# Kernel tuning notes

Hardware: AMD Instinct MI355X
Metric: run time of the kernel (lower is better)

Reference implementation:

```python
import jax, jax.numpy as jnp
import numpy as np

B, S, F = 2, 2048, 2048
H, D = 16, 128  # F == H * D


def setup_inputs() -> dict:
    key = jax.random.key(0)
    k1, k2, k3 = jax.random.split(key, 3)
    x = jax.random.normal(k1, (B, S, F), dtype=jnp.float32)
    # causal attention mask, broadcast over batch and heads
    mask = jnp.tril(jnp.ones((S, S), dtype=bool))[None, None, :, :]
    init_std = 0.02
    c_attn_kernel = jax.random.normal(k2, (F, 3 * F), dtype=jnp.float32) * init_std
    c_attn_bias = jnp.zeros((3 * F,), dtype=jnp.float32)
    c_proj_kernel = jax.random.normal(k3, (F, F), dtype=jnp.float32) * init_std
    c_proj_bias = jnp.zeros((F,), dtype=jnp.float32)
    return {
        "x": x,
        "mask": mask,
        "c_attn_kernel": c_attn_kernel,
        "c_attn_bias": c_attn_bias,
        "c_proj_kernel": c_proj_kernel,
        "c_proj_bias": c_proj_bias,
    }


def reference(x, mask, c_attn_kernel, c_attn_bias, c_proj_kernel, c_proj_bias):
    dtype = x.dtype
    # fused QKV projection: [B,S,F] @ [F,3F] -> [B,S,3F]
    hidden = jnp.einsum('bsf,fe->bse', x, c_attn_kernel) + c_attn_bias
    q, k, v = jnp.split(hidden, 3, axis=-1)
    split = lambda t: t.reshape(t.shape[:-1] + (H, D))  # [B,S,H,D]
    q, k, v = split(q), split(k), split(v)
    q = q / jnp.sqrt(jnp.asarray(D, dtype))
    scores = jnp.einsum('bqhd,bkhd->bhqk', q, k)  # [B,H,S,S]
    big_neg = jnp.finfo(dtype).min
    scores = jnp.where(mask[..., :S, :S], scores, big_neg)
    weights = jax.nn.softmax(scores, axis=-1)
    z = jnp.einsum('bhqk,bkhd->bqhd', weights, v)  # [B,S,H,D]
    merged = z.reshape(z.shape[:-2] + (F,))  # [B,S,F]
    out = jnp.einsum('bsf,fe->bse', merged, c_proj_kernel) + c_proj_bias
    return out
```

## Files before the change

### kernel.cpp

```cpp
#include <hip/hip_runtime.h>
#include <hip/hip_bf16.h>
#include <stdint.h>

typedef __attribute__((ext_vector_type(8))) __bf16 bf16x8;
typedef __attribute__((ext_vector_type(4))) __bf16 bf16x4;
typedef __attribute__((ext_vector_type(4))) float f32x4;

#define DEV __device__ __forceinline__

static constexpr int S = 2048, F = 2048, H = 16, D = 128;
static constexpr int KDIM = F;
static constexpr float QSCALE = 0.08838834764831845f;

DEV void gll16(const void* g, void* l) {
  __builtin_amdgcn_global_load_lds(
      (const __attribute__((address_space(1))) void*)g,
      (__attribute__((address_space(3))) void*)l, 16, 0, 0);
}

DEV f32x4 mfma16(bf16x8 a, bf16x8 b, f32x4 c) {
  return __builtin_amdgcn_mfma_f32_16x16x32_bf16(a, b, c, 0, 0, 0);
}

extern __shared__ char smem[];

__global__ void k_cvt(const float* __restrict__ in, __bf16* __restrict__ out) {
  int i = blockIdx.x * 256 + threadIdx.x;
  float4 v = reinterpret_cast<const float4*>(in)[i];
  bf16x4 o = {(__bf16)v.x, (__bf16)v.y, (__bf16)v.z, (__bf16)v.w};
  reinterpret_cast<bf16x4*>(out)[i] = o;
}

__global__ void k_transpose(const float* __restrict__ in, __bf16* __restrict__ out,
                            int rows, int cols) {
  __shared__ float t[64][65];
  const int c0 = blockIdx.x * 64, r0 = blockIdx.y * 64;
  const int tx = threadIdx.x & 63, ty = threadIdx.x >> 6;
#pragma unroll
  for (int i = 0; i < 64; i += 4)
    t[ty + i][tx] = in[(size_t)(r0 + ty + i) * cols + c0 + tx];
  __syncthreads();
#pragma unroll
  for (int i = 0; i < 64; i += 4)
    out[(size_t)(c0 + ty + i) * rows + r0 + tx] = (__bf16)t[tx][ty + i];
}

template <int EPI>
__global__ __launch_bounds__(512, 2) void k_gemm_tb(
    const __bf16* __restrict__ A, const __bf16* __restrict__ Bt,
    const float* __restrict__ bias,
    __bf16* __restrict__ qo, __bf16* __restrict__ ko, __bf16* __restrict__ vo,
    float* __restrict__ fo, int nbx) {
  const int tid = threadIdx.x;
  const int lane = tid & 63, wid = tid >> 6;
  const int wm = wid >> 2, wn = wid & 3;
  const int ln = lane & 15, lm = lane >> 4;

  const int q8 = gridDim.x >> 3;
  const int lin = (blockIdx.x & 7) * q8 + (blockIdx.x >> 3);
  const int bx = lin % nbx, by = lin / nbx;
  const int mBase = by * 128, nBase = bx * 256;

  int srcA[2], dstA[2], srcB[4], dstB[4];
#pragma unroll
  for (int j = 0; j < 2; ++j) {
    int c = j * 512 + tid, r = c >> 3, cc = c & 7;
    srcA[j] = r * KDIM + ((cc ^ (r & 7)) << 3);
    dstA[j] = j * 8192 + wid * 1024;
  }
#pragma unroll
  for (int j = 0; j < 4; ++j) {
    int c = j * 512 + tid, r = c >> 3, cc = c & 7;
    srcB[j] = r * KDIM + ((cc ^ (r & 7)) << 3);
    dstB[j] = 16384 + j * 8192 + wid * 1024;
  }
  const __bf16* Ab = A + (size_t)mBase * KDIM;
  const __bf16* Bb = Bt + (size_t)nBase * KDIM;

  int loA[2], loB[2];
#pragma unroll
  for (int ks = 0; ks < 2; ++ks) {
    int slot = (ks * 4 + lm) ^ (ln & 7);
    loA[ks] = (wm * 64 + ln) * 128 + slot * 16;
    loB[ks] = 16384 + (wn * 64 + ln) * 128 + slot * 16;
  }

  f32x4 acc[4][4] = {};
  constexpr int NT = KDIM / 64;

#pragma unroll
  for (int j = 0; j < 2; ++j) gll16(Ab + srcA[j], smem + dstA[j]);
#pragma unroll
  for (int j = 0; j < 4; ++j) gll16(Bb + srcB[j], smem + dstB[j]);
#pragma unroll
  for (int j = 0; j < 2; ++j) gll16(Ab + 64 + srcA[j], smem + 49152 + dstA[j]);
#pragma unroll
  for (int j = 0; j < 4; ++j) gll16(Bb + 64 + srcB[j], smem + 49152 + dstB[j]);
  asm volatile("s_waitcnt vmcnt(6)" ::: "memory");
  __builtin_amdgcn_s_barrier();
  __builtin_amdgcn_sched_barrier(0);

  for (int t = 0; t < NT; ++t) {
    const char* cbuf = smem + (t % 3) * 49152;
    char* nbuf = smem + ((t + 2) % 3) * 49152;
    const __bf16* Asrc = Ab + (t + 2) * 64;
    const __bf16* Bsrc = Bb + (t + 2) * 64;
    const bool pf = (t + 2 < NT);

    bf16x8 af0[4], bf0[4];
#pragma unroll
    for (int mi = 0; mi < 4; ++mi)
      af0[mi] = *reinterpret_cast<const bf16x8*>(cbuf + mi * 2048 + loA[0]);
#pragma unroll
    for (int ni = 0; ni < 4; ++ni)
      bf0[ni] = *reinterpret_cast<const bf16x8*>(cbuf + ni * 2048 + loB[0]);
    if (pf) {
      gll16(Asrc + srcA[0], nbuf + dstA[0]);
      gll16(Asrc + srcA[1], nbuf + dstA[1]);
      gll16(Bsrc + srcB[0], nbuf + dstB[0]);
    }
    __builtin_amdgcn_s_setprio(1);
#pragma unroll
    for (int mi = 0; mi < 4; ++mi)
#pragma unroll
      for (int ni = 0; ni < 4; ++ni)
        acc[mi][ni] = mfma16(af0[mi], bf0[ni], acc[mi][ni]);
    __builtin_amdgcn_s_setprio(0);

    bf16x8 af1[4], bf1[4];
#pragma unroll
    for (int mi = 0; mi < 4; ++mi)
      af1[mi] = *reinterpret_cast<const bf16x8*>(cbuf + mi * 2048 + loA[1]);
#pragma unroll
    for (int ni = 0; ni < 4; ++ni)
      bf1[ni] = *reinterpret_cast<const bf16x8*>(cbuf + ni * 2048 + loB[1]);
    if (pf) {
      gll16(Bsrc + srcB[1], nbuf + dstB[1]);
      gll16(Bsrc + srcB[2], nbuf + dstB[2]);
      gll16(Bsrc + srcB[3], nbuf + dstB[3]);
    }
    __builtin_amdgcn_s_setprio(1);
#pragma unroll
    for (int mi = 0; mi < 4; ++mi)
#pragma unroll
      for (int ni = 0; ni < 4; ++ni)
        acc[mi][ni] = mfma16(af1[mi], bf1[ni], acc[mi][ni]);
    __builtin_amdgcn_s_setprio(0);

    if (t < NT - 2)
      asm volatile("s_waitcnt vmcnt(6) lgkmcnt(0)" ::: "memory");
    else
      asm volatile("s_waitcnt vmcnt(0) lgkmcnt(0)" ::: "memory");
    __builtin_amdgcn_s_barrier();
    __builtin_amdgcn_sched_barrier(0);
  }

  if (EPI == 0) {
    const int sec = nBase >> 11;
#pragma unroll
    for (int mi = 0; mi < 4; ++mi) {
      const int grow = mBase + wm * 64 + mi * 16 + lm * 4;
      const int b = grow >> 11, s0 = grow & 2047;
#pragma unroll
      for (int ni = 0; ni < 4; ++ni) {
        const int gcol = nBase + wn * 64 + ni * 16 + ln;
        const float bv = bias[gcol];
        const int h = (gcol >> 7) & 15, d = gcol & 127;
        const int bh = b * H + h;
        if (sec == 0) {
#pragma unroll
          for (int r = 0; r < 4; ++r)
            qo[((size_t)bh * S + s0 + r) * D + d] = (__bf16)((acc[mi][ni][r] + bv) * QSCALE);
        } else if (sec == 1) {
#pragma unroll
          for (int r = 0; r < 4; ++r)
            ko[((size_t)bh * S + s0 + r) * D + d] = (__bf16)(acc[mi][ni][r] + bv);
        } else {
          bf16x4 pv = {(__bf16)(acc[mi][ni][0] + bv), (__bf16)(acc[mi][ni][1] + bv),
                       (__bf16)(acc[mi][ni][2] + bv), (__bf16)(acc[mi][ni][3] + bv)};
          *reinterpret_cast<bf16x4*>(vo + ((size_t)bh * D + d) * S + s0) = pv;
        }
      }
    }
  } else {
#pragma unroll
    for (int mi = 0; mi < 4; ++mi) {
      const int grow = mBase + wm * 64 + mi * 16 + lm * 4;
#pragma unroll
      for (int ni = 0; ni < 4; ++ni) {
        const int gcol = nBase + wn * 64 + ni * 16 + ln;
        const float bv = bias[gcol];
#pragma unroll
        for (int r = 0; r < 4; ++r)
          fo[(size_t)(grow + r) * F + gcol] = acc[mi][ni][r] + bv;
      }
    }
  }
}

__global__ __launch_bounds__(256, 2) void k_attn(
    const __bf16* __restrict__ qb, const __bf16* __restrict__ kb,
    const __bf16* __restrict__ vtb, __bf16* __restrict__ zb) {
  const int lane = threadIdx.x & 63, w = threadIdx.x >> 6;
  const int lm = lane >> 4, ln = lane & 15;
  const int blk = blockIdx.x;
  const int bh = blk & 31;
  const int qt = 15 - (blk >> 5);
  const int qw = qt * 128 + w * 32;

  const __bf16* qp = qb + (size_t)bh * S * D;
  const __bf16* kp = kb + (size_t)bh * S * D;
  const __bf16* vp = vtb + (size_t)bh * D * S;
  char* pw = smem + 65536 + w * 4096;

  int ksrc[4], kdst[4], vsrc[4], vdst[4];
#pragma unroll
  for (int j = 0; j < 4; ++j) {
    int c = (w * 4 + j) * 64 + lane;
    int kr = c >> 4, kps = (c & 15) ^ (kr & 7);
    ksrc[j] = kr * D + kps * 8;
    kdst[j] = (w * 4 + j) * 1024;
    int vr = c >> 3, vps = (c & 7) ^ (vr & 7);
    vsrc[j] = vr * S + vps * 8;
    vdst[j] = 16384 + (w * 4 + j) * 1024;
  }

  bf16x8 qf[2][4];
#pragma unroll
  for (int mi = 0; mi < 2; ++mi)
#pragma unroll
    for (int kf = 0; kf < 4; ++kf)
      qf[mi][kf] = *reinterpret_cast<const bf16x8*>(qp + (qw + mi * 16 + ln) * D + kf * 32 + lm * 8);

  f32x4 Oa[2][8] = {};
  float mrow[2][4], lrow[2][4];
#pragma unroll
  for (int mi = 0; mi < 2; ++mi)
#pragma unroll
    for (int r = 0; r < 4; ++r) { mrow[mi][r] = -3.0e38f; lrow[mi][r] = 0.0f; }

  const int ktEnd = 2 * qt + 1;

#pragma unroll
  for (int j = 0; j < 4; ++j) gll16(kp + ksrc[j], smem + kdst[j]);
#pragma unroll
  for (int j = 0; j < 4; ++j) gll16(vp + vsrc[j], smem + vdst[j]);
  asm volatile("s_waitcnt vmcnt(0)" ::: "memory");
  __builtin_amdgcn_s_barrier();
  __builtin_amdgcn_sched_barrier(0);

  for (int kt = 0; kt <= ktEnd; ++kt) {
    const int kv0 = kt * 64;
    const int cur = kt & 1;

    if (kt < ktEnd) {
      const int nk = (kt + 1) * 64;
      char* nbuf = smem + (cur ^ 1) * 32768;
#pragma unroll
      for (int j = 0; j < 4; ++j) gll16(kp + (size_t)nk * D + ksrc[j], nbuf + kdst[j]);
#pragma unroll
      for (int j = 0; j < 4; ++j) gll16(vp + nk + vsrc[j], nbuf + vdst[j] - 16384 + 16384);
    }

    if (kv0 <= qw + 31) {
      const char* Kb = smem + cur * 32768;
      const char* Vb = Kb + 16384;
      const bool diag = (kv0 + 63 > qw);

      f32x4 sacc[2][4] = {};
#pragma unroll
      for (int kf = 0; kf < 4; ++kf) {
        bf16x8 kfr[4];
#pragma unroll
        for (int ni = 0; ni < 4; ++ni) {
          int row = ni * 16 + ln;
          int ch = (kf * 4 + lm) ^ (row & 7);
          kfr[ni] = *reinterpret_cast<const bf16x8*>(Kb + row * 256 + ch * 16);
        }
        __builtin_amdgcn_s_setprio(1);
#pragma unroll
        for (int mi = 0; mi < 2; ++mi)
#pragma unroll
          for (int ni = 0; ni < 4; ++ni)
            sacc[mi][ni] = mfma16(qf[mi][kf], kfr[ni], sacc[mi][ni]);
        __builtin_amdgcn_s_setprio(0);
      }

      if (diag) {
#pragma unroll
        for (int ni = 0; ni < 4; ++ni) {
          int c = kv0 + ni * 16 + ln;
#pragma unroll
          for (int mi = 0; mi < 2; ++mi) {
            int q0r = qw + mi * 16 + lm * 4;
#pragma unroll
            for (int r = 0; r < 4; ++r)
              if (c > q0r + r) sacc[mi][ni][r] = -1e30f;
          }
        }
      }

#pragma unroll
      for (int mi = 0; mi < 2; ++mi)
#pragma unroll
        for (int r = 0; r < 4; ++r) {
          float mx = fmaxf(fmaxf(sacc[mi][0][r], sacc[mi][1][r]),
                           fmaxf(sacc[mi][2][r], sacc[mi][3][r]));
          mx = fmaxf(mx, __shfl_xor(mx, 1, 64));
          mx = fmaxf(mx, __shfl_xor(mx, 2, 64));
          mx = fmaxf(mx, __shfl_xor(mx, 4, 64));
          mx = fmaxf(mx, __shfl_xor(mx, 8, 64));
          float mnew = fmaxf(mrow[mi][r], mx);
          float corr = __expf(mrow[mi][r] - mnew);
          mrow[mi][r] = mnew;
          float rs = 0.0f;
#pragma unroll
          for (int ni = 0; ni < 4; ++ni) {
            float p = __expf(sacc[mi][ni][r] - mnew);
            sacc[mi][ni][r] = p;
            rs += p;
          }
          lrow[mi][r] = lrow[mi][r] * corr + rs;
#pragma unroll
          for (int ni = 0; ni < 8; ++ni) Oa[mi][ni][r] *= corr;
        }

#pragma unroll
      for (int mi = 0; mi < 2; ++mi)
#pragma unroll
        for (int ni = 0; ni < 4; ++ni)
#pragma unroll
          for (int r = 0; r < 4; ++r) {
            int row = mi * 16 + lm * 4 + r;
            int bo = (row * 128 + (ni * 16 + ln) * 2) ^ ((row & 7) << 4);
            *reinterpret_cast<__bf16*>(pw + bo) = (__bf16)sacc[mi][ni][r];
          }

      asm volatile("s_waitcnt lgkmcnt(0)" ::: "memory");
      __builtin_amdgcn_sched_barrier(0);

#pragma unroll
      for (int kf = 0; kf < 2; ++kf) {
        bf16x8 pfr[2], vfr[8];
#pragma unroll
        for (int mi = 0; mi < 2; ++mi) {
          int row = mi * 16 + ln;
          int ch = (kf * 4 + lm) ^ (row & 7);
          pfr[mi] = *reinterpret_cast<const bf16x8*>(pw + row * 128 + ch * 16);
        }
#pragma unroll
        for (int ni = 0; ni < 8; ++ni) {
          int row = ni * 16 + ln;
          int ch = (kf * 4 + lm) ^ (row & 7);
          vfr[ni] = *reinterpret_cast<const bf16x8*>(Vb + row * 128 + ch * 16);
        }
        __builtin_amdgcn_s_setprio(1);
#pragma unroll
        for (int mi = 0; mi < 2; ++mi)
#pragma unroll
          for (int ni = 0; ni < 8; ++ni)
            Oa[mi][ni] = mfma16(pfr[mi], vfr[ni], Oa[mi][ni]);
        __builtin_amdgcn_s_setprio(0);
      }
    }

    asm volatile("s_waitcnt vmcnt(0) lgkmcnt(0)" ::: "memory");
    __builtin_amdgcn_s_barrier();
    __builtin_amdgcn_sched_barrier(0);
  }

#pragma unroll
  for (int mi = 0; mi < 2; ++mi)
#pragma unroll
    for (int r = 0; r < 4; ++r) {
      float ls = lrow[mi][r];
      ls += __shfl_xor(ls, 1, 64);
      ls += __shfl_xor(ls, 2, 64);
      ls += __shfl_xor(ls, 4, 64);
      ls += __shfl_xor(ls, 8, 64);
      lrow[mi][r] = 1.0f / ls;
    }
  const int b = bh >> 4, h = bh & 15;
#pragma unroll
  for (int mi = 0; mi < 2; ++mi)
#pragma unroll
    for (int ni = 0; ni < 8; ++ni) {
      int d = ni * 16 + ln;
#pragma unroll
      for (int r = 0; r < 4; ++r) {
        int qrow = qw + mi * 16 + lm * 4 + r;
        zb[(size_t)(b * S + qrow) * F + h * D + d] = (__bf16)(Oa[mi][ni][r] * lrow[mi][r]);
      }
    }
}

extern "C" void kernel_launch(void* const* d_in, const int* in_sizes, int n_in,
                              void* d_out, int out_size, void* d_ws, size_t ws_size,
                              hipStream_t stream) {
  const float* x = (const float*)d_in[0];
  const float* w_attn = (const float*)d_in[2];
  const float* b_attn = (const float*)d_in[3];
  const float* w_proj = (const float*)d_in[4];
  const float* b_proj = (const float*)d_in[5];
  float* out = (float*)d_out;

  char* ws = (char*)d_ws;
  __bf16* xb    = (__bf16*)(ws + 0);
  __bf16* wqkv  = (__bf16*)(ws + 16777216);
  __bf16* wpro  = (__bf16*)(ws + 41943040);
  __bf16* qb    = (__bf16*)(ws + 50331648);
  __bf16* kb    = (__bf16*)(ws + 67108864);
  __bf16* vtb   = (__bf16*)(ws + 83886080);
  __bf16* zb    = xb;

  (void)hipFuncSetAttribute((const void*)k_gemm_tb<0>,
                            hipFuncAttributeMaxDynamicSharedMemorySize, 147456);
  (void)hipFuncSetAttribute((const void*)k_gemm_tb<1>,
                            hipFuncAttributeMaxDynamicSharedMemorySize, 147456);
  (void)hipFuncSetAttribute((const void*)k_attn,
                            hipFuncAttributeMaxDynamicSharedMemorySize, 81920);

  k_cvt<<<8192, 256, 0, stream>>>(x, xb);
  k_transpose<<<dim3(96, 32), 256, 0, stream>>>(w_attn, wqkv, 2048, 6144);
  k_transpose<<<dim3(32, 32), 256, 0, stream>>>(w_proj, wpro, 2048, 2048);
  k_gemm_tb<0><<<768, 512, 147456, stream>>>(xb, wqkv, b_attn, qb, kb, vtb, nullptr, 24);
  k_attn<<<512, 256, 81920, stream>>>(qb, kb, vtb, zb);
  k_gemm_tb<1><<<256, 512, 147456, stream>>>(zb, wpro, b_proj, nullptr, nullptr, nullptr, out, 8);
}
```

Before: 274.5 us.

## Use dedicated 256x384-tile QKV GEMM kernel with one wave of blocks

After: 275.1 us. Within noise of the previous version (+0.2%).

```diff
diff --git a/kernel.cpp b/kernel.cpp
--- a/kernel.cpp
+++ b/kernel.cpp
@@ -45,12 +45,136 @@
     out[(size_t)(c0 + ty + i) * rows + r0 + tx] = (__bf16)t[tx][ty + i];
 }
 
-template <int EPI>
-__global__ __launch_bounds__(512, 2) void k_gemm_tb(
+__global__ __launch_bounds__(512, 2) void k_qkv(
     const __bf16* __restrict__ A, const __bf16* __restrict__ Bt,
     const float* __restrict__ bias,
-    __bf16* __restrict__ qo, __bf16* __restrict__ ko, __bf16* __restrict__ vo,
-    float* __restrict__ fo, int nbx) {
+    __bf16* __restrict__ qo, __bf16* __restrict__ ko, __bf16* __restrict__ vo) {
+  const int tid = threadIdx.x;
+  const int lane = tid & 63, wid = tid >> 6;
+  const int wm = wid >> 2, wn = wid & 3;
+  const int ln = lane & 15, lm = lane >> 4;
+
+  const int lin = (blockIdx.x & 7) * 32 + (blockIdx.x >> 3);
+  const int by = lin >> 4, bx = lin & 15;
+  const int mBase = by * 256, nBase = bx * 384;
+
+  const int r0 = tid >> 3, cc = tid & 7;
+  const int src0 = r0 * KDIM + ((cc ^ (r0 & 7)) << 3);
+  const __bf16* Ab = A + (size_t)mBase * KDIM + src0;
+  const __bf16* Bb = Bt + (size_t)nBase * KDIM + src0;
+  const int dstBase = wid * 1024;
+
+  int rA[2], rB[2];
+#pragma unroll
+  for (int ks = 0; ks < 2; ++ks) {
+    const int slot = (ks * 4 + lm) ^ (ln & 7);
+    rA[ks] = (wm * 128 + ln) * 128 + slot * 16;
+    rB[ks] = 32768 + (wn * 96 + ln) * 128 + slot * 16;
+  }
+
+  f32x4 acc[8][6] = {};
+  constexpr int NT = KDIM / 64;
+
+#pragma unroll
+  for (int j = 0; j < 4; ++j) gll16(Ab + j * 131072, smem + j * 8192 + dstBase);
+#pragma unroll
+  for (int j = 0; j < 6; ++j) gll16(Bb + j * 131072, smem + 32768 + j * 8192 + dstBase);
+  asm volatile("s_waitcnt vmcnt(0)" ::: "memory");
+  __builtin_amdgcn_s_barrier();
+  __builtin_amdgcn_sched_barrier(0);
+
+  for (int t = 0; t < NT; ++t) {
+    const int cur = t & 1;
+    const char* cb = smem + cur * 81920;
+    char* nb = smem + (cur ^ 1) * 81920;
+    const __bf16* An = Ab + (t + 1) * 64;
+    const __bf16* Bn = Bb + (t + 1) * 64;
+    const bool pf = (t + 1 < NT);
+
+    {
+      bf16x8 a[8], b[6];
+#pragma unroll
+      for (int mi = 0; mi < 8; ++mi)
+        a[mi] = *reinterpret_cast<const bf16x8*>(cb + rA[0] + mi * 2048);
+#pragma unroll
+      for (int ni = 0; ni < 6; ++ni)
+        b[ni] = *reinterpret_cast<const bf16x8*>(cb + rB[0] + ni * 2048);
+      if (pf) {
+#pragma unroll
+        for (int j = 0; j < 4; ++j) gll16(An + j * 131072, nb + j * 8192 + dstBase);
+#pragma unroll
+        for (int j = 0; j < 2; ++j) gll16(Bn + j * 131072, nb + 32768 + j * 8192 + dstBase);
+      }
+      asm volatile("s_waitcnt lgkmcnt(0)" ::: "memory");
+      __builtin_amdgcn_sched_barrier(0);
+      __builtin_amdgcn_s_setprio(1);
+#pragma unroll
+      for (int ni = 0; ni < 6; ++ni)
+#pragma unroll
+        for (int mi = 0; mi < 8; ++mi)
+          acc[mi][ni] = mfma16(a[mi], b[ni], acc[mi][ni]);
+      __builtin_amdgcn_s_setprio(0);
+    }
+
+    {
+      bf16x8 a[8], b[6];
+#pragma unroll
+      for (int mi = 0; mi < 8; ++mi)
+        a[mi] = *reinterpret_cast<const bf16x8*>(cb + rA[1] + mi * 2048);
+#pragma unroll
+      for (int ni = 0; ni < 6; ++ni)
+        b[ni] = *reinterpret_cast<const bf16x8*>(cb + rB[1] + ni * 2048);
+      if (pf) {
+#pragma unroll
+        for (int j = 2; j < 6; ++j) gll16(Bn + j * 131072, nb + 32768 + j * 8192 + dstBase);
+      }
+      asm volatile("s_waitcnt lgkmcnt(0)" ::: "memory");
+      __builtin_amdgcn_sched_barrier(0);
+      __builtin_amdgcn_s_setprio(1);
+#pragma unroll
+      for (int ni = 0; ni < 6; ++ni)
+#pragma unroll
+        for (int mi = 0; mi < 8; ++mi)
+          acc[mi][ni] = mfma16(a[mi], b[ni], acc[mi][ni]);
+      __builtin_amdgcn_s_setprio(0);
+    }
+
+    asm volatile("s_waitcnt vmcnt(0)" ::: "memory");
+    __builtin_amdgcn_s_barrier();
+    __builtin_amdgcn_sched_barrier(0);
+  }
+
+#pragma unroll
+  for (int mi = 0; mi < 8; ++mi) {
+    const int grow = mBase + wm * 128 + mi * 16 + lm * 4;
+    const int b = grow >> 11, s0 = grow & 2047;
+#pragma unroll
+    for (int ni = 0; ni < 6; ++ni) {
+      const int gcol = nBase + wn * 96 + ni * 16 + ln;
+      const float bv = bias[gcol];
+      const int sec = gcol >> 11;
+      const int h = (gcol >> 7) & 15, d = gcol & 127;
+      const int bh = b * H + h;
+      if (sec == 0) {
+#pragma unroll
+        for (int r = 0; r < 4; ++r)
+          qo[((size_t)bh * S + s0 + r) * D + d] = (__bf16)((acc[mi][ni][r] + bv) * QSCALE);
+      } else if (sec == 1) {
+#pragma unroll
+        for (int r = 0; r < 4; ++r)
+          ko[((size_t)bh * S + s0 + r) * D + d] = (__bf16)(acc[mi][ni][r] + bv);
+      } else {
+        bf16x4 pv = {(__bf16)(acc[mi][ni][0] + bv), (__bf16)(acc[mi][ni][1] + bv),
+                     (__bf16)(acc[mi][ni][2] + bv), (__bf16)(acc[mi][ni][3] + bv)};
+        *reinterpret_cast<bf16x4*>(vo + ((size_t)bh * D + d) * S + s0) = pv;
+      }
+    }
+  }
+}
+
+__global__ __launch_bounds__(512, 2) void k_proj(
+    const __bf16* __restrict__ A, const __bf16* __restrict__ Bt,
+    const float* __restrict__ bias, float* __restrict__ fo, int nbx) {
   const int tid = threadIdx.x;
   const int lane = tid & 63, wid = tid >> 6;
   const int wm = wid >> 2, wn = wid & 3;
@@ -155,45 +279,16 @@
     __builtin_amdgcn_sched_barrier(0);
   }
 
-  if (EPI == 0) {
-    const int sec = nBase >> 11;
-#pragma unroll
-    for (int mi = 0; mi < 4; ++mi) {
-      const int grow = mBase + wm * 64 + mi * 16 + lm * 4;
-      const int b = grow >> 11, s0 = grow & 2047;
-#pragma unroll
-      for (int ni = 0; ni < 4; ++ni) {
-        const int gcol = nBase + wn * 64 + ni * 16 + ln;
-        const float bv = bias[gcol];
-        const int h = (gcol >> 7) & 15, d = gcol & 127;
-        const int bh = b * H + h;
-        if (sec == 0) {
-#pragma unroll
-          for (int r = 0; r < 4; ++r)
-            qo[((size_t)bh * S + s0 + r) * D + d] = (__bf16)((acc[mi][ni][r] + bv) * QSCALE);
-        } else if (sec == 1) {
-#pragma unroll
-          for (int r = 0; r < 4; ++r)
-            ko[((size_t)bh * S + s0 + r) * D + d] = (__bf16)(acc[mi][ni][r] + bv);
-        } else {
-          bf16x4 pv = {(__bf16)(acc[mi][ni][0] + bv), (__bf16)(acc[mi][ni][1] + bv),
-                       (__bf16)(acc[mi][ni][2] + bv), (__bf16)(acc[mi][ni][3] + bv)};
-          *reinterpret_cast<bf16x4*>(vo + ((size_t)bh * D + d) * S + s0) = pv;
-        }
-      }
-    }
-  } else {
-#pragma unroll
-    for (int mi = 0; mi < 4; ++mi) {
-      const int grow = mBase + wm * 64 + mi * 16 + lm * 4;
-#pragma unroll
-      for (int ni = 0; ni < 4; ++ni) {
-        const int gcol = nBase + wn * 64 + ni * 16 + ln;
-        const float bv = bias[gcol];
-#pragma unroll
-        for (int r = 0; r < 4; ++r)
-          fo[(size_t)(grow + r) * F + gcol] = acc[mi][ni][r] + bv;
-      }
+#pragma unroll
+  for (int mi = 0; mi < 4; ++mi) {
+    const int grow = mBase + wm * 64 + mi * 16 + lm * 4;
+#pragma unroll
+    for (int ni = 0; ni < 4; ++ni) {
+      const int gcol = nBase + wn * 64 + ni * 16 + ln;
+      const float bv = bias[gcol];
+#pragma unroll
+      for (int r = 0; r < 4; ++r)
+        fo[(size_t)(grow + r) * F + gcol] = acc[mi][ni][r] + bv;
     }
   }
 }
@@ -259,7 +354,7 @@
 #pragma unroll
       for (int j = 0; j < 4; ++j) gll16(kp + (size_t)nk * D + ksrc[j], nbuf + kdst[j]);
 #pragma unroll
-      for (int j = 0; j < 4; ++j) gll16(vp + nk + vsrc[j], nbuf + vdst[j] - 16384 + 16384);
+      for (int j = 0; j < 4; ++j) gll16(vp + nk + vsrc[j], nbuf + vdst[j]);
     }
 
     if (kv0 <= qw + 31) {
@@ -413,9 +508,9 @@
   __bf16* vtb   = (__bf16*)(ws + 83886080);
   __bf16* zb    = xb;
 
-  (void)hipFuncSetAttribute((const void*)k_gemm_tb<0>,
-                            hipFuncAttributeMaxDynamicSharedMemorySize, 147456);
-  (void)hipFuncSetAttribute((const void*)k_gemm_tb<1>,
+  (void)hipFuncSetAttribute((const void*)k_qkv,
+                            hipFuncAttributeMaxDynamicSharedMemorySize, 163840);
+  (void)hipFuncSetAttribute((const void*)k_proj,
                             hipFuncAttributeMaxDynamicSharedMemorySize, 147456);
   (void)hipFuncSetAttribute((const void*)k_attn,
                             hipFuncAttributeMaxDynamicSharedMemorySize, 81920);
@@ -423,7 +518,7 @@
   k_cvt<<<8192, 256, 0, stream>>>(x, xb);
   k_transpose<<<dim3(96, 32), 256, 0, stream>>>(w_attn, wqkv, 2048, 6144);
   k_transpose<<<dim3(32, 32), 256, 0, stream>>>(w_proj, wpro, 2048, 2048);
-  k_gemm_tb<0><<<768, 512, 147456, stream>>>(xb, wqkv, b_attn, qb, kb, vtb, nullptr, 24);
+  k_qkv<<<256, 512, 163840, stream>>>(xb, wqkv, b_attn, qb, kb, vtb);
   k_attn<<<512, 256, 81920, stream>>>(qb, kb, vtb, zb);
-  k_gemm_tb<1><<<256, 512, 147456, stream>>>(zb, wpro, b_proj, nullptr, nullptr, nullptr, out, 8);
-}
+  k_proj<<<256, 512, 147456, stream>>>(zb, wpro, b_proj, out, 8);
+}
```

## Template GEMM on tile sizes, use 256x384 QKV tiles with double buffering

Applied to the files above, without the earlier changes.

Measured after the change: 266.8 us. 2.8% less time.

```diff
diff --git a/kernel.cpp b/kernel.cpp
--- a/kernel.cpp
+++ b/kernel.cpp
@@ -45,126 +45,130 @@
     out[(size_t)(c0 + ty + i) * rows + r0 + tx] = (__bf16)t[tx][ty + i];
 }
 
-template <int EPI>
-__global__ __launch_bounds__(512, 2) void k_gemm_tb(
+template <int BM, int BN, int NBXL, int EPI>
+__global__ __launch_bounds__(512, 2) void k_gp(
     const __bf16* __restrict__ A, const __bf16* __restrict__ Bt,
     const float* __restrict__ bias,
     __bf16* __restrict__ qo, __bf16* __restrict__ ko, __bf16* __restrict__ vo,
-    float* __restrict__ fo, int nbx) {
+    float* __restrict__ fo) {
+  constexpr int MF = BM / 32;
+  constexpr int NF = BN / 64;
+  constexpr int NLA = BM / 64;
+  constexpr int NLB = BN / 64;
+  constexpr int NL = NLA + NLB;
+  constexpr int AOFF = BM * 128;
+  constexpr int BUFSZ = (BM + BN) * 128;
+  constexpr int NT = KDIM / 64;
+
   const int tid = threadIdx.x;
   const int lane = tid & 63, wid = tid >> 6;
   const int wm = wid >> 2, wn = wid & 3;
   const int ln = lane & 15, lm = lane >> 4;
 
-  const int q8 = gridDim.x >> 3;
-  const int lin = (blockIdx.x & 7) * q8 + (blockIdx.x >> 3);
-  const int bx = lin % nbx, by = lin / nbx;
-  const int mBase = by * 128, nBase = bx * 256;
-
-  int srcA[2], dstA[2], srcB[4], dstB[4];
-#pragma unroll
-  for (int j = 0; j < 2; ++j) {
-    int c = j * 512 + tid, r = c >> 3, cc = c & 7;
-    srcA[j] = r * KDIM + ((cc ^ (r & 7)) << 3);
-    dstA[j] = j * 8192 + wid * 1024;
+  const int lin = (blockIdx.x & 7) * 32 + (blockIdx.x >> 3);
+  const int by = lin >> NBXL, bx = lin & ((1 << NBXL) - 1);
+  const int mBase = by * BM, nBase = bx * BN;
+
+  const int r0 = tid >> 3, cc = tid & 7;
+  const int src0 = r0 * KDIM + ((cc ^ (r0 & 7)) << 3);
+  const __bf16* Ab = A + (size_t)mBase * KDIM + src0;
+  const __bf16* Bb = Bt + (size_t)nBase * KDIM + src0;
+  const int dstBase = wid * 1024;
+
+  auto stage = [&](char* buf, int t) {
+    const __bf16* As = Ab + t * 64;
+    const __bf16* Bs = Bb + t * 64;
+#pragma unroll
+    for (int j = 0; j < NLA; ++j)
+      gll16(As + (size_t)j * 64 * KDIM, buf + j * 8192 + dstBase);
+#pragma unroll
+    for (int j = 0; j < NLB; ++j)
+      gll16(Bs + (size_t)j * 64 * KDIM, buf + AOFF + j * 8192 + dstBase);
+  };
+
+  int rA[2], rB[2];
+#pragma unroll
+  for (int ks = 0; ks < 2; ++ks) {
+    const int slot = (ks * 4 + lm) ^ (ln & 7);
+    rA[ks] = (wm * (BM / 2) + ln) * 128 + slot * 16;
+    rB[ks] = AOFF + (wn * (BN / 4) + ln) * 128 + slot * 16;
   }
-#pragma unroll
-  for (int j = 0; j < 4; ++j) {
-    int c = j * 512 + tid, r = c >> 3, cc = c & 7;
-    srcB[j] = r * KDIM + ((cc ^ (r & 7)) << 3);
-    dstB[j] = 16384 + j * 8192 + wid * 1024;
-  }
-  const __bf16* Ab = A + (size_t)mBase * KDIM;
-  const __bf16* Bb = Bt + (size_t)nBase * KDIM;
-
-  int loA[2], loB[2];
-#pragma unroll
-  for (int ks = 0; ks < 2; ++ks) {
-    int slot = (ks * 4 + lm) ^ (ln & 7);
-    loA[ks] = (wm * 64 + ln) * 128 + slot * 16;
-    loB[ks] = 16384 + (wn * 64 + ln) * 128 + slot * 16;
-  }
-
-  f32x4 acc[4][4] = {};
-  constexpr int NT = KDIM / 64;
-
-#pragma unroll
-  for (int j = 0; j < 2; ++j) gll16(Ab + srcA[j], smem + dstA[j]);
-#pragma unroll
-  for (int j = 0; j < 4; ++j) gll16(Bb + srcB[j], smem + dstB[j]);
-#pragma unroll
-  for (int j = 0; j < 2; ++j) gll16(Ab + 64 + srcA[j], smem + 49152 + dstA[j]);
-#pragma unroll
-  for (int j = 0; j < 4; ++j) gll16(Bb + 64 + srcB[j], smem + 49152 + dstB[j]);
-  asm volatile("s_waitcnt vmcnt(6)" ::: "memory");
+
+  f32x4 acc[MF][NF] = {};
+
+  stage(smem, 0);
+  stage(smem + BUFSZ, 1);
+  if constexpr (NL == 10) asm volatile("s_waitcnt vmcnt(10)" ::: "memory");
+  else                    asm volatile("s_waitcnt vmcnt(6)" ::: "memory");
   __builtin_amdgcn_s_barrier();
   __builtin_amdgcn_sched_barrier(0);
 
   for (int t = 0; t < NT; ++t) {
-    const char* cbuf = smem + (t % 3) * 49152;
-    char* nbuf = smem + ((t + 2) % 3) * 49152;
-    const __bf16* Asrc = Ab + (t + 2) * 64;
-    const __bf16* Bsrc = Bb + (t + 2) * 64;
-    const bool pf = (t + 2 < NT);
-
-    bf16x8 af0[4], bf0[4];
-#pragma unroll
-    for (int mi = 0; mi < 4; ++mi)
-      af0[mi] = *reinterpret_cast<const bf16x8*>(cbuf + mi * 2048 + loA[0]);
-#pragma unroll
-    for (int ni = 0; ni < 4; ++ni)
-      bf0[ni] = *reinterpret_cast<const bf16x8*>(cbuf + ni * 2048 + loB[0]);
-    if (pf) {
-      gll16(Asrc + srcA[0], nbuf + dstA[0]);
-      gll16(Asrc + srcA[1], nbuf + dstA[1]);
-      gll16(Bsrc + srcB[0], nbuf + dstB[0]);
-    }
-    __builtin_amdgcn_s_setprio(1);
-#pragma unroll
-    for (int mi = 0; mi < 4; ++mi)
-#pragma unroll
-      for (int ni = 0; ni < 4; ++ni)
-        acc[mi][ni] = mfma16(af0[mi], bf0[ni], acc[mi][ni]);
-    __builtin_amdgcn_s_setprio(0);
-
-    bf16x8 af1[4], bf1[4];
-#pragma unroll
-    for (int mi = 0; mi < 4; ++mi)
-      af1[mi] = *reinterpret_cast<const bf16x8*>(cbuf + mi * 2048 + loA[1]);
-#pragma unroll
-    for (int ni = 0; ni < 4; ++ni)
-      bf1[ni] = *reinterpret_cast<const bf16x8*>(cbuf + ni * 2048 + loB[1]);
-    if (pf) {
-      gll16(Bsrc + srcB[1], nbuf + dstB[1]);
-      gll16(Bsrc + srcB[2], nbuf + dstB[2]);
-      gll16(Bsrc + srcB[3], nbuf + dstB[3]);
-    }
-    __builtin_amdgcn_s_setprio(1);
-#pragma unroll
-    for (int mi = 0; mi < 4; ++mi)
-#pragma unroll
-      for (int ni = 0; ni < 4; ++ni)
-        acc[mi][ni] = mfma16(af1[mi], bf1[ni], acc[mi][ni]);
-    __builtin_amdgcn_s_setprio(0);
-
-    if (t < NT - 2)
-      asm volatile("s_waitcnt vmcnt(6) lgkmcnt(0)" ::: "memory");
-    else
-      asm volatile("s_waitcnt vmcnt(0) lgkmcnt(0)" ::: "memory");
-    __builtin_amdgcn_s_barrier();
-    __builtin_amdgcn_sched_barrier(0);
+    char* cb = smem + (t & 1) * BUFSZ;
+
+    {
+      bf16x8 a[MF], b[NF];
+#pragma unroll
+      for (int mi = 0; mi < MF; ++mi)
+        a[mi] = *reinterpret_cast<const bf16x8*>(cb + rA[0] + mi * 2048);
+#pragma unroll
+      for (int ni = 0; ni < NF; ++ni)
+        b[ni] = *reinterpret_cast<const bf16x8*>(cb + rB[0] + ni * 2048);
+      asm volatile("s_waitcnt lgkmcnt(0)" ::: "memory");
+      __builtin_amdgcn_sched_barrier(0);
+      __builtin_amdgcn_s_setprio(1);
+#pragma unroll
+      for (int ni = 0; ni < NF; ++ni)
+#pragma unroll
+        for (int mi = 0; mi < MF; ++mi)
+          acc[mi][ni] = mfma16(a[mi], b[ni], acc[mi][ni]);
+      __builtin_amdgcn_s_setprio(0);
+    }
+
+    {
+      bf16x8 a[MF], b[NF];
+#pragma unroll
+      for (int mi = 0; mi < MF; ++mi)
+        a[mi] = *reinterpret_cast<const bf16x8*>(cb + rA[1] + mi * 2048);
+#pragma unroll
+      for (int ni = 0; ni < NF; ++ni)
+        b[ni] = *reinterpret_cast<const bf16x8*>(cb + rB[1] + ni * 2048);
+      asm volatile("s_waitcnt lgkmcnt(0)" ::: "memory");
+      __builtin_amdgcn_sched_barrier(0);
+      __builtin_amdgcn_s_barrier();
+      if (t + 2 < NT) stage(cb, t + 2);
+      __builtin_amdgcn_sched_barrier(0);
+      __builtin_amdgcn_s_setprio(1);
+#pragma unroll
+      for (int ni = 0; ni < NF; ++ni)
+#pragma unroll
+        for (int mi = 0; mi < MF; ++mi)
+          acc[mi][ni] = mfma16(a[mi], b[ni], acc[mi][ni]);
+      __builtin_amdgcn_s_setprio(0);
+    }
+
+    if (t + 2 < NT) {
+      if constexpr (NL == 10) asm volatile("s_waitcnt vmcnt(10)" ::: "memory");
+      else                    asm volatile("s_waitcnt vmcnt(6)" ::: "memory");
+    } else if (t + 1 < NT) {
+      asm volatile("s_waitcnt vmcnt(0)" ::: "memory");
+    }
+    if (t + 1 < NT) {
+      __builtin_amdgcn_s_barrier();
+      __builtin_amdgcn_sched_barrier(0);
+    }
   }
 
   if (EPI == 0) {
-    const int sec = nBase >> 11;
-#pragma unroll
-    for (int mi = 0; mi < 4; ++mi) {
-      const int grow = mBase + wm * 64 + mi * 16 + lm * 4;
+#pragma unroll
+    for (int mi = 0; mi < MF; ++mi) {
+      const int grow = mBase + wm * (BM / 2) + mi * 16 + lm * 4;
       const int b = grow >> 11, s0 = grow & 2047;
 #pragma unroll
-      for (int ni = 0; ni < 4; ++ni) {
-        const int gcol = nBase + wn * 64 + ni * 16 + ln;
+      for (int ni = 0; ni < NF; ++ni) {
+        const int gcol = nBase + wn * (BN / 4) + ni * 16 + ln;
         const float bv = bias[gcol];
+        const int sec = gcol >> 11;
         const int h = (gcol >> 7) & 15, d = gcol & 127;
         const int bh = b * H + h;
         if (sec == 0) {
@@ -184,11 +188,11 @@
     }
   } else {
 #pragma unroll
-    for (int mi = 0; mi < 4; ++mi) {
-      const int grow = mBase + wm * 64 + mi * 16 + lm * 4;
-#pragma unroll
-      for (int ni = 0; ni < 4; ++ni) {
-        const int gcol = nBase + wn * 64 + ni * 16 + ln;
+    for (int mi = 0; mi < MF; ++mi) {
+      const int grow = mBase + wm * (BM / 2) + mi * 16 + lm * 4;
+#pragma unroll
+      for (int ni = 0; ni < NF; ++ni) {
+        const int gcol = nBase + wn * (BN / 4) + ni * 16 + ln;
         const float bv = bias[gcol];
 #pragma unroll
         for (int r = 0; r < 4; ++r)
@@ -259,7 +263,7 @@
 #pragma unroll
       for (int j = 0; j < 4; ++j) gll16(kp + (size_t)nk * D + ksrc[j], nbuf + kdst[j]);
 #pragma unroll
-      for (int j = 0; j < 4; ++j) gll16(vp + nk + vsrc[j], nbuf + vdst[j] - 16384 + 16384);
+      for (int j = 0; j < 4; ++j) gll16(vp + nk + vsrc[j], nbuf + vdst[j]);
     }
 
     if (kv0 <= qw + 31) {
@@ -413,17 +417,17 @@
   __bf16* vtb   = (__bf16*)(ws + 83886080);
   __bf16* zb    = xb;
 
-  (void)hipFuncSetAttribute((const void*)k_gemm_tb<0>,
-                            hipFuncAttributeMaxDynamicSharedMemorySize, 147456);
-  (void)hipFuncSetAttribute((const void*)k_gemm_tb<1>,
-                            hipFuncAttributeMaxDynamicSharedMemorySize, 147456);
+  (void)hipFuncSetAttribute((const void*)k_gp<256, 384, 4, 0>,
+                            hipFuncAttributeMaxDynamicSharedMemorySize, 163840);
+  (void)hipFuncSetAttribute((const void*)k_gp<128, 256, 3, 1>,
+                            hipFuncAttributeMaxDynamicSharedMemorySize, 98304);
   (void)hipFuncSetAttribute((const void*)k_attn,
                             hipFuncAttributeMaxDynamicSharedMemorySize, 81920);
 
   k_cvt<<<8192, 256, 0, stream>>>(x, xb);
   k_transpose<<<dim3(96, 32), 256, 0, stream>>>(w_attn, wqkv, 2048, 6144);
   k_transpose<<<dim3(32, 32), 256, 0, stream>>>(w_proj, wpro, 2048, 2048);
-  k_gemm_tb<0><<<768, 512, 147456, stream>>>(xb, wqkv, b_attn, qb, kb, vtb, nullptr, 24);
+  k_gp<256, 384, 4, 0><<<256, 512, 163840, stream>>>(xb, wqkv, b_attn, qb, kb, vtb, nullptr);
   k_attn<<<512, 256, 81920, stream>>>(qb, kb, vtb, zb);
-  k_gemm_tb<1><<<256, 512, 147456, stream>>>(zb, wpro, b_proj, nullptr, nullptr, nullptr, out, 8);
-}
+  k_gp<128, 256, 3, 1><<<256, 512, 98304, stream>>>(zb, wpro, b_proj, nullptr, nullptr, nullptr, out);
+}
```
